# Kernel tuning notes

Hardware: AMD Instinct MI355X
Metric: run time of the kernel (lower is better)

The kernel has to match this reference:

```python
import jax, jax.numpy as jnp
import numpy as np

N, C, H, W = 8, 256, 128, 128   # images, AE-error channels, feature map size
A = 3                            # anchors per location (3 aspect ratios)
G = 64                           # GT boxes per image
STRIDE = 8
ANCHOR_SIZE = 32.0
ASPECT_RATIOS = (0.5, 1.0, 2.0)
UNK_CLASS = 80
D = 64                           # density_dim


def make_anchors():
    # detectron2 DefaultAnchorGenerator: cell anchors + grid shifts, (H, W, A) order, A fastest
    r = jnp.asarray(ASPECT_RATIOS, jnp.float32)
    w = ANCHOR_SIZE / jnp.sqrt(r)
    h = ANCHOR_SIZE * jnp.sqrt(r)
    cell = jnp.stack([-w / 2, -h / 2, w / 2, h / 2], axis=1)          # [A,4]
    sx = jnp.arange(W, dtype=jnp.float32) * STRIDE
    sy = jnp.arange(H, dtype=jnp.float32) * STRIDE
    yy, xx = jnp.meshgrid(sy, sx, indexing='ij')
    shifts = jnp.stack([xx, yy, xx, yy], axis=-1).reshape(-1, 4)      # [H*W,4]
    return (shifts[:, None, :] + cell[None, :, :]).reshape(-1, 4)     # [H*W*A,4]


def pairwise_iou(boxes, anchors):
    # boxes [G,4], anchors [R,4] -> [G,R]
    area_b = (boxes[:, 2] - boxes[:, 0]) * (boxes[:, 3] - boxes[:, 1])
    area_a = (anchors[:, 2] - anchors[:, 0]) * (anchors[:, 3] - anchors[:, 1])
    lt = jnp.maximum(boxes[:, None, :2], anchors[None, :, :2])
    rb = jnp.minimum(boxes[:, None, 2:], anchors[None, :, 2:])
    wh = jnp.clip(rb - lt, 0.0)
    inter = wh[..., 0] * wh[..., 1]
    return inter / jnp.maximum(area_b[:, None] + area_a[None, :] - inter, 1e-9)


def setup_inputs() -> dict:
    key = jax.random.key(0)
    k = jax.random.split(key, 9)
    err = jax.random.normal(k[0], (N, C, H, W), jnp.float32)
    err_map = jax.random.normal(k[1], (N, 1, H, W), jnp.float32)
    cxy = jax.random.uniform(k[2], (N, G, 2), minval=0.0, maxval=float(H * STRIDE))
    wh = jax.random.uniform(k[3], (N, G, 2), minval=16.0, maxval=128.0)
    gt_boxes = jnp.concatenate([cxy - wh / 2, cxy + wh / 2], axis=-1)
    gt_classes = jax.random.randint(k[4], (N, G), 0, 81, dtype=jnp.int32)
    w1 = jax.random.normal(k[5], (1, D), jnp.float32) * 0.5
    b1 = jnp.zeros((D,), jnp.float32)
    w2 = jax.random.normal(k[6], (D, D // 2), jnp.float32) * (1.0 / np.sqrt(D))
    b2 = jnp.zeros((D // 2,), jnp.float32)
    w3 = jax.random.normal(k[7], (D // 2, 1), jnp.float32) * (1.0 / np.sqrt(D // 2))
    b3 = jnp.zeros((1,), jnp.float32)
    return dict(err=err, err_map=err_map, gt_boxes=gt_boxes, w1=w1, b1=b1,
                w2=w2, b2=b2, w3=w3, b3=b3, gt_classes=gt_classes)


def reference(err, err_map, gt_boxes, w1, b1, w2, b2, w3, b3, gt_classes):
    # loss_ae: mean of squared flattened per-anchor errors (mean is permutation invariant)
    loss_ae = jnp.mean(err ** 2)

    # density head on every error-map pixel: Linear(1,D)-ReLU-Linear(D,D/2)-ReLU-Linear(D/2,1)
    pix = err_map.transpose(0, 2, 3, 1).reshape(N, H * W)              # [N,M]
    hmid = jax.nn.relu(pix[..., None] * w1[0] + b1)                    # [N,M,D]
    hmid = jax.nn.relu(jnp.einsum('nmd,de->nme', hmid, w2) + b2)       # [N,M,D/2]
    p_unk = (jnp.einsum('nme,eo->nmo', hmid, w3) + b3)[..., 0]         # [N,M]

    # anchor matching (torch.no_grad in original)
    anchors = make_anchors()                                           # [R,4]

    def match_one(boxes_i, classes_i):
        iou = pairwise_iou(boxes_i, anchors)                           # [G,R]
        idxs = jnp.argmax(iou, axis=0)                                 # per-anchor best GT
        return classes_i[idxs]                                         # [R]

    matched_classes = jax.vmap(match_one)(jax.lax.stop_gradient(gt_boxes), gt_classes)
    unk = (matched_classes == UNK_CLASS)                               # [N,R]
    mask = jnp.any(unk.reshape(N, H * W, A), axis=2).astype(jnp.float32)  # [N,M]

    # BCE with logits, mean reduction (stable form)
    loss_density = jnp.mean(jnp.logaddexp(0.0, p_unk) - p_unk * mask)
    return jnp.stack([loss_ae, loss_density])
```

## Files before the change

### kernel.cpp

```cpp
#include <hip/hip_runtime.h>
#include <math.h>

#define NIMG 8
#define HDIM 128
#define WDIM 128
#define MPIX (HDIM*WDIM)
#define GNUM 64
#define DDIM 64
#define EDIM 32
#define UNK_CLASS 80
#define N_ERR4 8388608
#define NBLK 2048
#define AE_BLOCKS 1536
#define AE_STRIDE (AE_BLOCKS*256)

__global__ __launch_bounds__(256) void fused_kernel(
    const float* __restrict__ err,
    const float* __restrict__ err_map,
    const float* __restrict__ gt_boxes,
    const float* __restrict__ w1,
    const float* __restrict__ b1,
    const float* __restrict__ w2,
    const float* __restrict__ b2,
    const float* __restrict__ w3,
    const float* __restrict__ b3,
    const int*   __restrict__ gt_classes,
    float* __restrict__ ws)
{
    const int t = threadIdx.x;
    const int b = blockIdx.x;
    float partial = 0.0f;

    __shared__ float4 sboxes[GNUM];
    __shared__ int    scls[GNUM];
    __shared__ float  sw1[DDIM], sb1[DDIM], sb2[EDIM], sw3[EDIM];
    __shared__ __align__(16) float sw2t[DDIM*EDIM];
    __shared__ float red[4];

    if ((b & 3) == 0) {
        const int db = b >> 2;
        const int n  = db >> 6;
        const int m  = ((db & 63) << 8) | t;

        if (t < GNUM)               sboxes[t]      = ((const float4*)gt_boxes)[n*GNUM + t];
        else if (t < 2*GNUM)        scls[t-GNUM]   = gt_classes[n*GNUM + (t-GNUM)];
        else if (t < 2*GNUM+DDIM) { sw1[t-128] = w1[t-128]; sb1[t-128] = b1[t-128]; }
        else if (t < 2*GNUM+DDIM+EDIM) { sb2[t-192] = b2[t-192]; sw3[t-192] = w3[t-192]; }
        for (int i = t; i < DDIM*EDIM; i += 256)
            sw2t[i] = w2[(i & 63)*EDIM + (i >> 6)];
        __syncthreads();

        const float cx = (float)(m & (WDIM-1)) * 8.0f;
        const float cy = (float)(m >> 7) * 8.0f;
        const float s05 = sqrtf(0.5f), s2 = sqrtf(2.0f);
        const float hw0 = 0.5f*(32.0f/s05), hh0 = 0.5f*(32.0f*s05);
        const float hw1 = 16.0f,            hh1 = 16.0f;
        const float hw2 = 0.5f*(32.0f/s2),  hh2 = 0.5f*(32.0f*s2);

        const float ax1[3] = {cx-hw0, cx-hw1, cx-hw2};
        const float ay1[3] = {cy-hh0, cy-hh1, cy-hh2};
        const float ax2[3] = {cx+hw0, cx+hw1, cx+hw2};
        const float ay2[3] = {cy+hh0, cy+hh1, cy+hh2};
        float areaA[3];
        #pragma unroll
        for (int a = 0; a < 3; ++a) areaA[a] = (ax2[a]-ax1[a])*(ay2[a]-ay1[a]);

        float bi[3] = {-1.f,-1.f,-1.f}, bd[3] = {1.f,1.f,1.f};
        int   idx[3] = {0,0,0};

        for (int g = 0; g < GNUM; ++g) {
            const float4 bx = sboxes[g];
            const float areaB = (bx.z-bx.x)*(bx.w-bx.y);
            #pragma unroll
            for (int a = 0; a < 3; ++a) {
                float lx = fmaxf(bx.x, ax1[a]), ly = fmaxf(bx.y, ay1[a]);
                float rx = fminf(bx.z, ax2[a]), ry = fminf(bx.w, ay2[a]);
                float iw = fmaxf(rx-lx, 0.f),   ih = fmaxf(ry-ly, 0.f);
                float inter = iw*ih;
                float dn = fmaxf(areaB + areaA[a] - inter, 1e-9f);
                if (inter*bd[a] > bi[a]*dn) { bi[a]=inter; bd[a]=dn; idx[a]=g; }
            }
        }
        const bool unk = (scls[idx[0]] == UNK_CLASS) |
                         (scls[idx[1]] == UNK_CLASS) |
                         (scls[idx[2]] == UNK_CLASS);
        const float mask = unk ? 1.0f : 0.0f;

        const float xv = err_map[(n << 14) + m];
        float h1[DDIM];
        #pragma unroll
        for (int d = 0; d < DDIM; ++d)
            h1[d] = fmaxf(fmaf(xv, sw1[d], sb1[d]), 0.0f);

        float p = b3[0];
        for (int e = 0; e < EDIM; ++e) {
            const float4* wr = (const float4*)&sw2t[e << 6];
            float a0=0.f, a1=0.f, a2=0.f, a3=0.f;
            #pragma unroll
            for (int q = 0; q < 16; ++q) {
                float4 wv = wr[q];
                a0 = fmaf(h1[4*q+0], wv.x, a0);
                a1 = fmaf(h1[4*q+1], wv.y, a1);
                a2 = fmaf(h1[4*q+2], wv.z, a2);
                a3 = fmaf(h1[4*q+3], wv.w, a3);
            }
            float acc = sb2[e] + ((a0+a1)+(a2+a3));
            p = fmaf(fmaxf(acc, 0.0f), sw3[e], p);
        }

        partial = fmaxf(p, 0.0f) + log1pf(expf(-fabsf(p))) - p*mask;
    } else {
        const int ae = b - (b >> 2) - 1;
        const float4* e4 = (const float4*)err;
        float s0 = 0.f, s1 = 0.f;
        for (int i = ae*256 + t; i < N_ERR4; i += AE_STRIDE) {
            float4 v = e4[i];
            s0 = fmaf(v.x, v.x, s0);
            s1 = fmaf(v.y, v.y, s1);
            s0 = fmaf(v.z, v.z, s0);
            s1 = fmaf(v.w, v.w, s1);
        }
        partial = s0 + s1;
    }

    float s = partial;
    #pragma unroll
    for (int off = 32; off > 0; off >>= 1) s += __shfl_xor(s, off, 64);
    if ((t & 63) == 0) red[t >> 6] = s;
    __syncthreads();
    if (t == 0) ws[b] = (red[0]+red[1]) + (red[2]+red[3]);
}

__global__ __launch_bounds__(256) void finalize_kernel(const float* __restrict__ ws,
                                                       float* __restrict__ out)
{
    const int t = threadIdx.x;
    float sd = 0.f, sa = 0.f;
    for (int i = t; i < NBLK; i += 256) {
        float v = ws[i];
        if ((i & 3) == 0) sd += v; else sa += v;
    }
    #pragma unroll
    for (int off = 32; off > 0; off >>= 1) {
        sd += __shfl_xor(sd, off, 64);
        sa += __shfl_xor(sa, off, 64);
    }
    __shared__ float rd[4], ra[4];
    if ((t & 63) == 0) { rd[t >> 6] = sd; ra[t >> 6] = sa; }
    __syncthreads();
    if (t == 0) {
        out[0] = ((ra[0]+ra[1])+(ra[2]+ra[3])) * (1.0f/33554432.0f);
        out[1] = ((rd[0]+rd[1])+(rd[2]+rd[3])) * (1.0f/131072.0f);
    }
}

extern "C" void kernel_launch(void* const* d_in, const int* in_sizes, int n_in,
                              void* d_out, int out_size, void* d_ws, size_t ws_size,
                              hipStream_t stream) {
    const float* err        = (const float*)d_in[0];
    const float* err_map    = (const float*)d_in[1];
    const float* gt_boxes   = (const float*)d_in[2];
    const float* w1         = (const float*)d_in[3];
    const float* b1         = (const float*)d_in[4];
    const float* w2         = (const float*)d_in[5];
    const float* b2         = (const float*)d_in[6];
    const float* w3         = (const float*)d_in[7];
    const float* b3         = (const float*)d_in[8];
    const int*   gt_classes = (const int*)d_in[9];
    float* out = (float*)d_out;
    float* ws  = (float*)d_ws;

    fused_kernel<<<NBLK, 256, 0, stream>>>(err, err_map, gt_boxes, w1, b1, w2, b2,
                                           w3, b3, gt_classes, ws);
    finalize_kernel<<<1, 256, 0, stream>>>(ws, out);
}
```

Baseline: 255.3 us.

## Issue all AE loads up front in every block and overlap density work

Every block now starts by issuing eight independent float4 loads of the AE error tensor (a fixed slice per thread, 4096 blocks), then the first 512 blocks also run the density/anchor-matching path while those loads are in flight. This replaces the grid-strided loop over dedicated AE blocks and the 1-in-4 interleaving of density blocks. The aim is to raise memory-level parallelism and hide the latency of the compute-heavy density path behind the bandwidth-bound reduction. In exchange, density blocks hold more registers and are concentrated at the start of the grid, which may cause load imbalance.

```diff
diff --git a/kernel.cpp b/kernel.cpp
--- a/kernel.cpp
+++ b/kernel.cpp
@@ -10,9 +10,9 @@
 #define EDIM 32
 #define UNK_CLASS 80
 #define N_ERR4 8388608
-#define NBLK 2048
-#define AE_BLOCKS 1536
-#define AE_STRIDE (AE_BLOCKS*256)
+#define NBLK 4096
+#define DBLK 512
+#define AE_THREADS (NBLK*256)
 
 __global__ __launch_bounds__(256) void fused_kernel(
     const float* __restrict__ err,
@@ -29,18 +29,38 @@
 {
     const int t = threadIdx.x;
     const int b = blockIdx.x;
-    float partial = 0.0f;
 
     __shared__ float4 sboxes[GNUM];
     __shared__ int    scls[GNUM];
     __shared__ float  sw1[DDIM], sb1[DDIM], sb2[EDIM], sw3[EDIM];
     __shared__ __align__(16) float sw2t[DDIM*EDIM];
-    __shared__ float red[4];
+    __shared__ float redA[4], redD[4];
 
-    if ((b & 3) == 0) {
-        const int db = b >> 2;
-        const int n  = db >> 6;
-        const int m  = ((db & 63) << 8) | t;
+    const float4* __restrict__ e4 = (const float4*)err;
+    const int gtid = (b << 8) | t;
+    float4 v0 = e4[gtid + 0*AE_THREADS];
+    float4 v1 = e4[gtid + 1*AE_THREADS];
+    float4 v2 = e4[gtid + 2*AE_THREADS];
+    float4 v3 = e4[gtid + 3*AE_THREADS];
+    float4 v4 = e4[gtid + 4*AE_THREADS];
+    float4 v5 = e4[gtid + 5*AE_THREADS];
+    float4 v6 = e4[gtid + 6*AE_THREADS];
+    float4 v7 = e4[gtid + 7*AE_THREADS];
+    float s0, s1, s2, s3;
+    s0 = v0.x*v0.x; s1 = v0.y*v0.y; s2 = v0.z*v0.z; s3 = v0.w*v0.w;
+    s0 = fmaf(v1.x,v1.x,s0); s1 = fmaf(v1.y,v1.y,s1); s2 = fmaf(v1.z,v1.z,s2); s3 = fmaf(v1.w,v1.w,s3);
+    s0 = fmaf(v2.x,v2.x,s0); s1 = fmaf(v2.y,v2.y,s1); s2 = fmaf(v2.z,v2.z,s2); s3 = fmaf(v2.w,v2.w,s3);
+    s0 = fmaf(v3.x,v3.x,s0); s1 = fmaf(v3.y,v3.y,s1); s2 = fmaf(v3.z,v3.z,s2); s3 = fmaf(v3.w,v3.w,s3);
+    s0 = fmaf(v4.x,v4.x,s0); s1 = fmaf(v4.y,v4.y,s1); s2 = fmaf(v4.z,v4.z,s2); s3 = fmaf(v4.w,v4.w,s3);
+    s0 = fmaf(v5.x,v5.x,s0); s1 = fmaf(v5.y,v5.y,s1); s2 = fmaf(v5.z,v5.z,s2); s3 = fmaf(v5.w,v5.w,s3);
+    s0 = fmaf(v6.x,v6.x,s0); s1 = fmaf(v6.y,v6.y,s1); s2 = fmaf(v6.z,v6.z,s2); s3 = fmaf(v6.w,v6.w,s3);
+    s0 = fmaf(v7.x,v7.x,s0); s1 = fmaf(v7.y,v7.y,s1); s2 = fmaf(v7.z,v7.z,s2); s3 = fmaf(v7.w,v7.w,s3);
+    float aePart = (s0+s1) + (s2+s3);
+    float dPart = 0.0f;
+
+    if (b < DBLK) {
+        const int n  = b >> 6;
+        const int m  = ((b & 63) << 8) | t;
 
         if (t < GNUM)               sboxes[t]      = ((const float4*)gt_boxes)[n*GNUM + t];
         else if (t < 2*GNUM)        scls[t-GNUM]   = gt_classes[n*GNUM + (t-GNUM)];
@@ -52,10 +72,10 @@
 
         const float cx = (float)(m & (WDIM-1)) * 8.0f;
         const float cy = (float)(m >> 7) * 8.0f;
-        const float s05 = sqrtf(0.5f), s2 = sqrtf(2.0f);
+        const float s05 = sqrtf(0.5f), s2r = sqrtf(2.0f);
         const float hw0 = 0.5f*(32.0f/s05), hh0 = 0.5f*(32.0f*s05);
         const float hw1 = 16.0f,            hh1 = 16.0f;
-        const float hw2 = 0.5f*(32.0f/s2),  hh2 = 0.5f*(32.0f*s2);
+        const float hw2 = 0.5f*(32.0f/s2r), hh2 = 0.5f*(32.0f*s2r);
 
         const float ax1[3] = {cx-hw0, cx-hw1, cx-hw2};
         const float ay1[3] = {cy-hh0, cy-hh1, cy-hh2};
@@ -108,45 +128,37 @@
             p = fmaf(fmaxf(acc, 0.0f), sw3[e], p);
         }
 
-        partial = fmaxf(p, 0.0f) + log1pf(expf(-fabsf(p))) - p*mask;
-    } else {
-        const int ae = b - (b >> 2) - 1;
-        const float4* e4 = (const float4*)err;
-        float s0 = 0.f, s1 = 0.f;
-        for (int i = ae*256 + t; i < N_ERR4; i += AE_STRIDE) {
-            float4 v = e4[i];
-            s0 = fmaf(v.x, v.x, s0);
-            s1 = fmaf(v.y, v.y, s1);
-            s0 = fmaf(v.z, v.z, s0);
-            s1 = fmaf(v.w, v.w, s1);
-        }
-        partial = s0 + s1;
+        dPart = fmaxf(p, 0.0f) + log1pf(expf(-fabsf(p))) - p*mask;
     }
 
-    float s = partial;
+    float x = aePart, y = dPart;
     #pragma unroll
-    for (int off = 32; off > 0; off >>= 1) s += __shfl_xor(s, off, 64);
-    if ((t & 63) == 0) red[t >> 6] = s;
+    for (int off = 32; off > 0; off >>= 1) {
+        x += __shfl_xor(x, off, 64);
+        y += __shfl_xor(y, off, 64);
+    }
+    if ((t & 63) == 0) { redA[t >> 6] = x; redD[t >> 6] = y; }
     __syncthreads();
-    if (t == 0) ws[b] = (red[0]+red[1]) + (red[2]+red[3]);
+    if (t == 0) {
+        ws[b] = (redA[0]+redA[1]) + (redA[2]+redA[3]);
+        if (b < DBLK) ws[NBLK + b] = (redD[0]+redD[1]) + (redD[2]+redD[3]);
+    }
 }
 
 __global__ __launch_bounds__(256) void finalize_kernel(const float* __restrict__ ws,
                                                        float* __restrict__ out)
 {
     const int t = threadIdx.x;
-    float sd = 0.f, sa = 0.f;
-    for (int i = t; i < NBLK; i += 256) {
-        float v = ws[i];
-        if ((i & 3) == 0) sd += v; else sa += v;
-    }
+    float sa = 0.f, sd = 0.f;
+    for (int i = t; i < NBLK; i += 256) sa += ws[i];
+    for (int i = t; i < DBLK; i += 256) sd += ws[NBLK + i];
     #pragma unroll
     for (int off = 32; off > 0; off >>= 1) {
+        sa += __shfl_xor(sa, off, 64);
         sd += __shfl_xor(sd, off, 64);
-        sa += __shfl_xor(sa, off, 64);
     }
-    __shared__ float rd[4], ra[4];
-    if ((t & 63) == 0) { rd[t >> 6] = sd; ra[t >> 6] = sa; }
+    __shared__ float ra[4], rd[4];
+    if ((t & 63) == 0) { ra[t >> 6] = sa; rd[t >> 6] = sd; }
     __syncthreads();
     if (t == 0) {
         out[0] = ((ra[0]+ra[1])+(ra[2]+ra[3])) * (1.0f/33554432.0f);
```

After: 219.0 us. 1.17x faster.
